# Optimization experiments

Measured on AMD Instinct MI355X. Metric: run time of the kernel, lower is better.

The kernel has to match this reference:

```python
import jax, jax.numpy as jnp
import numpy as np

EMBED_DIM = 1024
NUM_HEADS = 16
HEAD_DIM = EMBED_DIM // NUM_HEADS


def setup_inputs() -> dict:
    key = jax.random.key(0)
    ks = jax.random.split(key, 5)
    B, T, C = 2, 2048, EMBED_DIM
    s_in = 1.0 / np.sqrt(C)
    x = jax.random.normal(ks[0], (B, T, C), dtype=jnp.float32)
    W_qkv = jax.random.normal(ks[1], (C, 3 * C), dtype=jnp.float32) * s_in
    b_qkv = jnp.zeros((3 * C,), dtype=jnp.float32)
    W_out = jax.random.normal(ks[2], (C, C), dtype=jnp.float32) * s_in
    b_out = jnp.zeros((C,), dtype=jnp.float32)
    return {"x": x, "W_qkv": W_qkv, "b_qkv": b_qkv, "W_out": W_out, "b_out": b_out}


def reference(x, W_qkv, b_qkv, W_out, b_out):
    B, T, C = x.shape
    H, D = NUM_HEADS, HEAD_DIM
    qkv = x @ W_qkv + b_qkv                      # [B,T,3C]
    qkv = qkv.reshape(B, T, 3, H, D)
    q = jnp.transpose(qkv[:, :, 0], (0, 2, 1, 3))  # [B,H,T,D]
    k = jnp.transpose(qkv[:, :, 1], (0, 2, 1, 3))
    v = jnp.transpose(qkv[:, :, 2], (0, 2, 1, 3))
    scores = jnp.einsum('bhtd,bhsd->bhts', q, k) / np.sqrt(D).astype(jnp.float32)
    attn = jax.nn.softmax(scores, axis=-1)
    ctx = jnp.einsum('bhts,bhsd->bhtd', attn, v)   # [B,H,T,D]
    ctx = jnp.transpose(ctx, (0, 2, 1, 3)).reshape(B, T, C)
    return ctx @ W_out + b_out
```

## Files before the change

kernel.cpp:

```cpp
#include <hip/hip_runtime.h>
#include <hip/hip_bf16.h>


typedef __attribute__((ext_vector_type(8)))  short short8;
typedef __attribute__((ext_vector_type(4)))  float floatx4;
typedef __attribute__((ext_vector_type(16))) float floatx16;

__device__ inline ushort f2bf(float f) {
    union { __hip_bfloat16 h; ushort u; } c; c.h = __float2bfloat16(f); return c.u;
}

__device__ inline uint cvt_pk_bf16(float a, float b) {
    uint r;
    asm("v_cvt_pk_bf16_f32 %0, %1, %2" : "=v"(r) : "v"(a), "v"(b));
    return r;
}

__device__ inline void gld16(const ushort* g, ushort* l) {
    __builtin_amdgcn_global_load_lds(
        (__attribute__((address_space(1))) void*)(g),
        (__attribute__((address_space(3))) void*)(l), 16, 0, 0);
}

__device__ inline void tile_transpose(const float* __restrict__ src, ushort* __restrict__ dst,
                                      int R, int C, int rt, int ct, int t, ushort* L)
{
    const int row = t >> 2, cc = (t & 3) * 16;
    const float* sp = src + (long)(rt * 64 + row) * C + ct * 64 + cc;
    ushort tmp[16];
    #pragma unroll
    for (int i = 0; i < 4; i++) {
        float4 v = *(const float4*)(sp + i * 4);
        tmp[i*4+0]=f2bf(v.x); tmp[i*4+1]=f2bf(v.y); tmp[i*4+2]=f2bf(v.z); tmp[i*4+3]=f2bf(v.w);
    }
    *(uint4*)&L[row * 72 + cc]     = *(uint4*)&tmp[0];
    *(uint4*)&L[row * 72 + cc + 8] = *(uint4*)&tmp[8];
    __syncthreads();
    const int c = t >> 2, rc = (t & 3) * 16;
    ushort o[16];
    #pragma unroll
    for (int j = 0; j < 16; j++) o[j] = L[(rc + j) * 72 + c];
    ushort* dp = dst + (long)(ct * 64 + c) * R + rt * 64 + rc;
    *(uint4*)dp       = *(uint4*)&o[0];
    *(uint4*)(dp + 8) = *(uint4*)&o[8];
}

__global__ __launch_bounds__(256) void prep_kernel(
    const float* __restrict__ x, const float* __restrict__ Wqkv, const float* __restrict__ Wout,
    ushort* __restrict__ xb, ushort* __restrict__ wqkvT, ushort* __restrict__ woutT)
{
    __shared__ __align__(16) ushort L[64 * 72];
    const int bid = blockIdx.x, t = threadIdx.x;
    if (bid < 2048) {
        long i = ((long)bid * 256 + t) * 8;
        float4 a = *(const float4*)(x + i);
        float4 b = *(const float4*)(x + i + 4);
        ushort tmp[8] = { f2bf(a.x), f2bf(a.y), f2bf(a.z), f2bf(a.w),
                          f2bf(b.x), f2bf(b.y), f2bf(b.z), f2bf(b.w) };
        *(uint4*)(xb + i) = *(uint4*)tmp;
    } else if (bid < 2048 + 768) {
        int idx = bid - 2048;
        tile_transpose(Wqkv, wqkvT, 1024, 3072, idx & 15, idx >> 4, t, L);
    } else {
        int idx = bid - 2048 - 768;
        tile_transpose(Wout, woutT, 1024, 1024, idx & 15, idx >> 4, t, L);
    }
}

#define QSCALE 0.18033688011112042f

__global__ __launch_bounds__(256) void qkv_gemm_kernel(
    const ushort* __restrict__ A, const ushort* __restrict__ Bt,
    const float* __restrict__ bias,
    ushort* __restrict__ qbuf, ushort* __restrict__ kbuf, ushort* __restrict__ vtG)
{
    __shared__ __align__(16) ushort SMEM[16384];
    ushort* Asb[2] = { SMEM,        SMEM + 4096 };
    ushort* Bsb[2] = { SMEM + 8192, SMEM + 12288 };

    const int t = threadIdx.x;
    const int w = t >> 6, lane = t & 63;
    const int r = lane & 15, qq = lane >> 4;
    const int wm = w >> 1, wn = w & 1;
    const int rowBase = blockIdx.y * 128, colBase = blockIdx.x * 128;

    const int g_row = lane >> 2, g_kc = (lane & 3) * 8;
    const ushort* aP0 = A  + (long)(rowBase +      w * 16 + g_row) * 1024 + g_kc;
    const ushort* aP1 = A  + (long)(rowBase + 64 + w * 16 + g_row) * 1024 + g_kc;
    const ushort* bP0 = Bt + (long)(colBase +      w * 16 + g_row) * 1024 + g_kc;
    const ushort* bP1 = Bt + (long)(colBase + 64 + w * 16 + g_row) * 1024 + g_kc;

    floatx4 acc[4][4] = {};

    for (int k0 = 0; k0 < 1024; k0 += 64) {
        #pragma unroll
        for (int kk = 0; kk < 2; kk++) {
            gld16(aP0 + k0 + kk * 32, &Asb[kk][(w * 16) * 32]);
            gld16(aP1 + k0 + kk * 32, &Asb[kk][(64 + w * 16) * 32]);
            gld16(bP0 + k0 + kk * 32, &Bsb[kk][(w * 16) * 32]);
            gld16(bP1 + k0 + kk * 32, &Bsb[kk][(64 + w * 16) * 32]);
        }
        __syncthreads();
        #pragma unroll
        for (int kk = 0; kk < 2; kk++) {
            short8 af[4], bf4[4];
            #pragma unroll
            for (int tm = 0; tm < 4; tm++) af[tm]  = *(const short8*)&Asb[kk][(wm * 64 + tm * 16 + r) * 32 + qq * 8];
            #pragma unroll
            for (int tn = 0; tn < 4; tn++) bf4[tn] = *(const short8*)&Bsb[kk][(wn * 64 + tn * 16 + r) * 32 + qq * 8];
            #pragma unroll
            for (int tm = 0; tm < 4; tm++)
                #pragma unroll
                for (int tn = 0; tn < 4; tn++)
                    acc[tm][tn] = __builtin_amdgcn_mfma_f32_16x16x32_bf16(af[tm], bf4[tn], acc[tm][tn], 0, 0, 0);
        }
        __syncthreads();
    }

    if (colBase < 2048) {
        #pragma unroll
        for (int tn = 0; tn < 4; tn++) {
            int col = colBase + wn * 64 + tn * 16 + r;
            float bvv = bias[col];
            #pragma unroll
            for (int tm = 0; tm < 4; tm++) {
                #pragma unroll
                for (int reg = 0; reg < 4; reg++) {
                    int row = rowBase + wm * 64 + tm * 16 + qq * 4 + reg;
                    float val = acc[tm][tn][reg] + bvv;
                    if (colBase < 1024) qbuf[(long)row * 1024 + col]        = f2bf(val * QSCALE);
                    else                kbuf[(long)row * 1024 + col - 1024] = f2bf(val);
                }
            }
        }
    } else {
        ushort* L = SMEM;
        #pragma unroll
        for (int hh = 0; hh < 2; hh++) {
            __syncthreads();
            if (wn == hh) {
                #pragma unroll
                for (int tn = 0; tn < 4; tn++) {
                    int vc = tn * 16 + r;
                    float bvv = bias[colBase + wn * 64 + vc];
                    #pragma unroll
                    for (int tm = 0; tm < 4; tm++) {
                        int row0 = wm * 64 + tm * 16 + qq * 4;
                        ushort q4[4] = { f2bf(acc[tm][tn][0] + bvv), f2bf(acc[tm][tn][1] + bvv),
                                         f2bf(acc[tm][tn][2] + bvv), f2bf(acc[tm][tn][3] + bvv) };
                        *(uint2*)&L[vc * 136 + row0] = *(uint2*)q4;
                    }
                }
            }
            __syncthreads();
            int d = t >> 2, tq = (t & 3) * 32;
            int h_loc = ((colBase - 2048) >> 6) + hh;
            long vtrow = (long)((rowBase >> 11) * 16 + h_loc) * 64 + d;
            ushort* dst = vtG + vtrow * 2048 + (rowBase & 2047) + tq;
            #pragma unroll
            for (int i = 0; i < 4; i++)
                *(uint4*)(dst + 8 * i) = *(uint4*)&L[d * 136 + tq + 8 * i];
        }
    }
}

__global__ __launch_bounds__(256) void out_gemm_kernel(
    const ushort* __restrict__ A, const ushort* __restrict__ Bt,
    const float* __restrict__ bias, float* __restrict__ out)
{
    __shared__ __align__(16) ushort As[2][128 * 32];
    __shared__ __align__(16) ushort Bs[2][64 * 32];

    const int t = threadIdx.x;
    const int w = t >> 6, lane = t & 63;
    const int r = lane & 15, qq = lane >> 4;
    const int wm = w >> 1, wn = w & 1;
    const int rowBase = blockIdx.y * 128, colBase = blockIdx.x * 64;

    const int g_row = lane >> 2, g_kc = (lane & 3) * 8;
    const ushort* aP0 = A  + (long)(rowBase +      w * 16 + g_row) * 1024 + g_kc;
    const ushort* aP1 = A  + (long)(rowBase + 64 + w * 16 + g_row) * 1024 + g_kc;
    const ushort* bP0 = Bt + (long)(colBase +      w * 16 + g_row) * 1024 + g_kc;

    floatx4 acc[4][2] = {};

    for (int k0 = 0; k0 < 1024; k0 += 64) {
        #pragma unroll
        for (int kk = 0; kk < 2; kk++) {
            gld16(aP0 + k0 + kk * 32, &As[kk][(w * 16) * 32]);
            gld16(aP1 + k0 + kk * 32, &As[kk][(64 + w * 16) * 32]);
            gld16(bP0 + k0 + kk * 32, &Bs[kk][(w * 16) * 32]);
        }
        __syncthreads();
        #pragma unroll
        for (int kk = 0; kk < 2; kk++) {
            short8 af[4], bf2[2];
            #pragma unroll
            for (int tm = 0; tm < 4; tm++) af[tm]  = *(const short8*)&As[kk][(wm * 64 + tm * 16 + r) * 32 + qq * 8];
            #pragma unroll
            for (int tn = 0; tn < 2; tn++) bf2[tn] = *(const short8*)&Bs[kk][(wn * 32 + tn * 16 + r) * 32 + qq * 8];
            #pragma unroll
            for (int tm = 0; tm < 4; tm++)
                #pragma unroll
                for (int tn = 0; tn < 2; tn++)
                    acc[tm][tn] = __builtin_amdgcn_mfma_f32_16x16x32_bf16(af[tm], bf2[tn], acc[tm][tn], 0, 0, 0);
        }
        __syncthreads();
    }

    #pragma unroll
    for (int tn = 0; tn < 2; tn++) {
        int col = colBase + wn * 32 + tn * 16 + r;
        float bvv = bias[col];
        #pragma unroll
        for (int tm = 0; tm < 4; tm++) {
            #pragma unroll
            for (int reg = 0; reg < 4; reg++) {
                int row = rowBase + wm * 64 + tm * 16 + qq * 4 + reg;
                out[(long)row * 1024 + col] = acc[tm][tn][reg] + bvv;
            }
        }
    }
}

__global__ __launch_bounds__(256) void attn_kernel(
    ushort* __restrict__ qbuf, const ushort* __restrict__ kbuf,
    const ushort* __restrict__ vt)
{
    __shared__ __align__(16) ushort SM[2][2][64 * 72];

    const int t = threadIdx.x;
    const int w = t >> 6, lane = t & 63;
    const int m32 = lane & 31, hi = lane >> 5;

    const int qt = blockIdx.x;
    const int bh = blockIdx.y;
    const int b = bh >> 4, h = bh & 15;
    const long qrow = (long)(b * 2048 + qt * 128 + w * 32 + m32);

    short8 qfrag[4];
    #pragma unroll
    for (int dc = 0; dc < 4; dc++)
        qfrag[dc] = *(const short8*)(qbuf + qrow * 1024 + h * 64 + dc * 16 + hi * 8);

    short8 vones;
    #pragma unroll
    for (int i = 0; i < 8; i++) vones[i] = (short)0x3F80;

    const int srow = t >> 2, scol = (t & 3) * 16;
    const ushort* kP = kbuf + (long)(b * 2048 + srow) * 1024 + h * 64 + scol;
    const ushort* vP = vt + (long)(bh * 64 + srow) * 2048 + scol;

    floatx16 o[2] = {};
    floatx16 lacc = {};

    uint4 kr0, kr1, vr0, vr1;

    kr0 = *(const uint4*)kP;  kr1 = *(const uint4*)(kP + 8);
    vr0 = *(const uint4*)vP;  vr1 = *(const uint4*)(vP + 8);
    {
        ushort* Ks = SM[0][0]; ushort* Vs = SM[0][1];
        *(uint4*)&Ks[srow * 72 + scol]     = kr0;
        *(uint4*)&Ks[srow * 72 + scol + 8] = kr1;
        *(uint4*)&Vs[srow * 72 + scol]     = vr0;
        *(uint4*)&Vs[srow * 72 + scol + 8] = vr1;
    }
    kr0 = *(const uint4*)(kP + 64 * 1024); kr1 = *(const uint4*)(kP + 64 * 1024 + 8);
    vr0 = *(const uint4*)(vP + 64);        vr1 = *(const uint4*)(vP + 64 + 8);
    __syncthreads();

    #pragma unroll 2
    for (int kt = 0; kt < 32; kt++) {
        ushort* Ks = SM[kt & 1][0];
        ushort* Vs = SM[kt & 1][1];

        if (kt < 31) {
            ushort* Kn = SM[(kt + 1) & 1][0];
            ushort* Vn = SM[(kt + 1) & 1][1];
            *(uint4*)&Kn[srow * 72 + scol]     = kr0;
            *(uint4*)&Kn[srow * 72 + scol + 8] = kr1;
            *(uint4*)&Vn[srow * 72 + scol]     = vr0;
            *(uint4*)&Vn[srow * 72 + scol + 8] = vr1;
            if (kt < 30) {
                const ushort* kp = kP + (long)(kt + 2) * 64 * 1024;
                const ushort* vp = vP + (kt + 2) * 64;
                kr0 = *(const uint4*)kp; kr1 = *(const uint4*)(kp + 8);
                vr0 = *(const uint4*)vp; vr1 = *(const uint4*)(vp + 8);
            }
        }

        floatx16 s[2] = {};
        __builtin_amdgcn_s_setprio(1);
        #pragma unroll
        for (int c = 0; c < 2; c++) {
            #pragma unroll
            for (int dc = 0; dc < 4; dc++) {
                short8 kf = *(const short8*)&Ks[(c * 32 + m32) * 72 + dc * 16 + hi * 8];
                s[c] = __builtin_amdgcn_mfma_f32_32x32x16_bf16(kf, qfrag[dc], s[c], 0, 0, 0);
            }
        }
        __builtin_amdgcn_s_setprio(0);

        uint pk[2][8];
        #pragma unroll
        for (int c = 0; c < 2; c++) {
            #pragma unroll
            for (int i = 0; i < 8; i++) {
                float p0 = __builtin_amdgcn_exp2f(s[c][2 * i]);
                float p1 = __builtin_amdgcn_exp2f(s[c][2 * i + 1]);
                pk[c][i] = cvt_pk_bf16(p0, p1);
            }
        }

        __builtin_amdgcn_s_setprio(1);
        #pragma unroll
        for (int c = 0; c < 2; c++) {
            #pragma unroll
            for (int kc = 0; kc < 2; kc++) {
                uint a0 = pk[c][4 * kc + 0], b0 = pk[c][4 * kc + 2];
                asm("v_permlane32_swap_b32 %0, %1" : "+v"(a0), "+v"(b0));
                uint a1 = pk[c][4 * kc + 1], b1 = pk[c][4 * kc + 3];
                asm("v_permlane32_swap_b32 %0, %1" : "+v"(a1), "+v"(b1));
                union { uint u[4]; short8 s8; } cv;
                cv.u[0] = a0; cv.u[1] = a1; cv.u[2] = b0; cv.u[3] = b1;
                #pragma unroll
                for (int dt = 0; dt < 2; dt++) {
                    short8 vf = *(const short8*)&Vs[(dt * 32 + m32) * 72 + c * 32 + kc * 16 + hi * 8];
                    o[dt] = __builtin_amdgcn_mfma_f32_32x32x16_bf16(vf, cv.s8, o[dt], 0, 0, 0);
                }
                lacc = __builtin_amdgcn_mfma_f32_32x32x16_bf16(vones, cv.s8, lacc, 0, 0, 0);
            }
        }
        __builtin_amdgcn_s_setprio(0);

        __syncthreads();
    }

    float inv = 1.f / lacc[0];

    #pragma unroll
    for (int dt = 0; dt < 2; dt++) {
        #pragma unroll
        for (int g = 0; g < 4; g++) {
            ushort tmp[4] = { f2bf(o[dt][4*g+0] * inv), f2bf(o[dt][4*g+1] * inv),
                              f2bf(o[dt][4*g+2] * inv), f2bf(o[dt][4*g+3] * inv) };
            *(uint2*)(qbuf + qrow * 1024 + h * 64 + dt * 32 + g * 8 + hi * 4) = *(uint2*)tmp;
        }
    }
}

extern "C" void kernel_launch(void* const* d_in, const int* in_sizes, int n_in,
                              void* d_out, int out_size, void* d_ws, size_t ws_size,
                              hipStream_t stream) {
    const float* x     = (const float*)d_in[0];
    const float* W_qkv = (const float*)d_in[1];
    const float* b_qkv = (const float*)d_in[2];
    const float* W_out = (const float*)d_in[3];
    const float* b_out = (const float*)d_in[4];
    float* out = (float*)d_out;

    ushort* qbuf  = (ushort*)d_ws;
    ushort* kbuf  = qbuf + (size_t)4096 * 1024;
    ushort* vt    = kbuf + (size_t)4096 * 1024;
    ushort* woutT = vt + (size_t)2048 * 2048;
    ushort* wqkvT = woutT + (size_t)1024 * 1024;

    ushort* xb    = (ushort*)d_out;

    dim3 blk(256);
    prep_kernel<<<3072, blk, 0, stream>>>(x, W_qkv, W_out, xb, wqkvT, woutT);
    qkv_gemm_kernel<<<dim3(24, 32), blk, 0, stream>>>(xb, wqkvT, b_qkv, qbuf, kbuf, vt);
    attn_kernel<<<dim3(16, 32), blk, 0, stream>>>(qbuf, kbuf, vt);
    out_gemm_kernel<<<dim3(16, 32), blk, 0, stream>>>(qbuf, woutT, b_out, out);
}
```

Baseline: 196.8 us.

## Split attention KV range across two wave groups per block and merge partials

```diff
diff --git a/kernel.cpp b/kernel.cpp
--- a/kernel.cpp
+++ b/kernel.cpp
@@ -223,20 +223,23 @@
     }
 }
 
-__global__ __launch_bounds__(256) void attn_kernel(
+__global__ __launch_bounds__(512, 4) void attn_kernel(
     ushort* __restrict__ qbuf, const ushort* __restrict__ kbuf,
     const ushort* __restrict__ vt)
 {
-    __shared__ __align__(16) ushort SM[2][2][64 * 72];
+    __shared__ __align__(16) ushort SM[2][2][2][64 * 72];
 
     const int t = threadIdx.x;
     const int w = t >> 6, lane = t & 63;
     const int m32 = lane & 31, hi = lane >> 5;
-
-    const int qt = blockIdx.x;
-    const int bh = blockIdx.y;
+    const int h2 = w >> 2, wq = w & 3;
+
+    const int id = blockIdx.x;
+    const int j = id >> 3;
+    const int bh = (id & 7) * 4 + (j >> 4);
+    const int qt = j & 15;
     const int b = bh >> 4, h = bh & 15;
-    const long qrow = (long)(b * 2048 + qt * 128 + w * 32 + m32);
+    const long qrow = (long)(b * 2048 + qt * 128 + wq * 32 + m32);
 
     short8 qfrag[4];
     #pragma unroll
@@ -247,9 +250,10 @@
     #pragma unroll
     for (int i = 0; i < 8; i++) vones[i] = (short)0x3F80;
 
-    const int srow = t >> 2, scol = (t & 3) * 16;
-    const ushort* kP = kbuf + (long)(b * 2048 + srow) * 1024 + h * 64 + scol;
-    const ushort* vP = vt + (long)(bh * 64 + srow) * 2048 + scol;
+    const int ts = t & 255;
+    const int srow = ts >> 2, scol = (ts & 3) * 16;
+    const ushort* kP = kbuf + (long)(b * 2048 + h2 * 1024 + srow) * 1024 + h * 64 + scol;
+    const ushort* vP = vt + (long)(bh * 64 + srow) * 2048 + h2 * 1024 + scol;
 
     floatx16 o[2] = {};
     floatx16 lacc = {};
@@ -259,7 +263,7 @@
     kr0 = *(const uint4*)kP;  kr1 = *(const uint4*)(kP + 8);
     vr0 = *(const uint4*)vP;  vr1 = *(const uint4*)(vP + 8);
     {
-        ushort* Ks = SM[0][0]; ushort* Vs = SM[0][1];
+        ushort* Ks = SM[h2][0][0]; ushort* Vs = SM[h2][0][1];
         *(uint4*)&Ks[srow * 72 + scol]     = kr0;
         *(uint4*)&Ks[srow * 72 + scol + 8] = kr1;
         *(uint4*)&Vs[srow * 72 + scol]     = vr0;
@@ -270,20 +274,20 @@
     __syncthreads();
 
     #pragma unroll 2
-    for (int kt = 0; kt < 32; kt++) {
-        ushort* Ks = SM[kt & 1][0];
-        ushort* Vs = SM[kt & 1][1];
-
-        if (kt < 31) {
-            ushort* Kn = SM[(kt + 1) & 1][0];
-            ushort* Vn = SM[(kt + 1) & 1][1];
+    for (int tt = 0; tt < 16; tt++) {
+        ushort* Ks = SM[h2][tt & 1][0];
+        ushort* Vs = SM[h2][tt & 1][1];
+
+        if (tt < 15) {
+            ushort* Kn = SM[h2][(tt + 1) & 1][0];
+            ushort* Vn = SM[h2][(tt + 1) & 1][1];
             *(uint4*)&Kn[srow * 72 + scol]     = kr0;
             *(uint4*)&Kn[srow * 72 + scol + 8] = kr1;
             *(uint4*)&Vn[srow * 72 + scol]     = vr0;
             *(uint4*)&Vn[srow * 72 + scol + 8] = vr1;
-            if (kt < 30) {
-                const ushort* kp = kP + (long)(kt + 2) * 64 * 1024;
-                const ushort* vp = vP + (kt + 2) * 64;
+            if (tt < 14) {
+                const ushort* kp = kP + (long)(tt + 2) * 64 * 1024;
+                const ushort* vp = vP + (tt + 2) * 64;
                 kr0 = *(const uint4*)kp; kr1 = *(const uint4*)(kp + 8);
                 vr0 = *(const uint4*)vp; vr1 = *(const uint4*)(vp + 8);
             }
@@ -336,15 +340,29 @@
         __syncthreads();
     }
 
-    float inv = 1.f / lacc[0];
-
-    #pragma unroll
-    for (int dt = 0; dt < 2; dt++) {
-        #pragma unroll
-        for (int g = 0; g < 4; g++) {
-            ushort tmp[4] = { f2bf(o[dt][4*g+0] * inv), f2bf(o[dt][4*g+1] * inv),
-                              f2bf(o[dt][4*g+2] * inv), f2bf(o[dt][4*g+3] * inv) };
-            *(uint2*)(qbuf + qrow * 1024 + h * 64 + dt * 32 + g * 8 + hi * 4) = *(uint2*)tmp;
+    float* OL = (float*)SM;
+    float* LL = OL + 4 * 2048;
+    if (h2 == 1) {
+        #pragma unroll
+        for (int dt = 0; dt < 2; dt++)
+            #pragma unroll
+            for (int i = 0; i < 16; i++)
+                OL[wq * 2048 + (dt * 16 + i) * 64 + lane] = o[dt][i];
+        LL[wq * 64 + lane] = lacc[0];
+    }
+    __syncthreads();
+    if (h2 == 0) {
+        float inv = 1.f / (lacc[0] + LL[wq * 64 + lane]);
+        #pragma unroll
+        for (int dt = 0; dt < 2; dt++) {
+            #pragma unroll
+            for (int i = 0; i < 16; i++) o[dt][i] += OL[wq * 2048 + (dt * 16 + i) * 64 + lane];
+            #pragma unroll
+            for (int g = 0; g < 4; g++) {
+                ushort tmp[4] = { f2bf(o[dt][4*g+0] * inv), f2bf(o[dt][4*g+1] * inv),
+                                  f2bf(o[dt][4*g+2] * inv), f2bf(o[dt][4*g+3] * inv) };
+                *(uint2*)(qbuf + qrow * 1024 + h * 64 + dt * 32 + g * 8 + hi * 4) = *(uint2*)tmp;
+            }
         }
     }
 }
@@ -370,6 +388,6 @@
     dim3 blk(256);
     prep_kernel<<<3072, blk, 0, stream>>>(x, W_qkv, W_out, xb, wqkvT, woutT);
     qkv_gemm_kernel<<<dim3(24, 32), blk, 0, stream>>>(xb, wqkvT, b_qkv, qbuf, kbuf, vt);
-    attn_kernel<<<dim3(16, 32), blk, 0, stream>>>(qbuf, kbuf, vt);
+    attn_kernel<<<512, dim3(512), 0, stream>>>(qbuf, kbuf, vt);
     out_gemm_kernel<<<dim3(16, 32), blk, 0, stream>>>(qbuf, woutT, b_out, out);
 }
```

Result: no change. 194.8 us (-1.0%).
